# Optimization experiments

Measured on AMD Instinct MI355X. Metric: run time of the kernel, lower is better.

The kernel has to match this reference:

```python
import jax, jax.numpy as jnp
import numpy as np

DK = 8.0          # sqrt(in_dim) with in_dim = 64
BN_SCALE = 1.0 / np.float32(np.sqrt(1.0 + 1e-5))  # eval-mode BatchNorm3d at init (mean=0, var=1, gamma=1, beta=0)


def conv3d(x, w, b):
    # x: [B,Cin,D1,D2,D3], w: [Cout,Cin,3,3,3], stride 1, padding 1 == SAME
    y = jax.lax.conv_general_dilated(
        x, w, window_strides=(1, 1, 1), padding='SAME',
        dimension_numbers=('NCDHW', 'OIDHW', 'NCDHW'))
    return y + b[None, :, None, None, None]


def axial(qm, km, vm):
    # qm/km/vm: [B,C,S,L,M]; attention over L with keys along M-contraction.
    # scores[b,c,s,i,j] = sum_m (q/dk)[...,i,m] * k[...,j,m]  -> [B,C,S,L,L]
    s = jnp.einsum('bcsim,bcsjm->bcsij', qm / DK, km)
    # torch nn.Softmax(dim=1) applied to [N,L,L] normalizes over the FIRST L axis (i)
    a = jax.nn.softmax(s, axis=-2)
    return jnp.einsum('bcsij,bcsjm->bcsim', a, vm)


def setup_inputs() -> dict:
    key = jax.random.key(0)
    ks = jax.random.split(key, 5)
    B, C, H, W, D = 2, 64, 64, 64, 64
    x = jax.random.normal(ks[0], (B, C, H, W, D), jnp.float32)
    Wq = jax.random.normal(ks[1], (C, C, 3, 3, 3), jnp.float32) * 0.02
    Wk = jax.random.normal(ks[2], (C, C, 3, 3, 3), jnp.float32) * 0.02
    Wv = jax.random.normal(ks[3], (C, C, 3, 3, 3), jnp.float32) * 0.02
    Wc = jax.random.normal(ks[4], (C, 3 * C, 3, 3, 3), jnp.float32) * 0.02
    z = jnp.zeros((C,), jnp.float32)
    return {"x": x, "Wq": Wq, "bq": z, "Wk": Wk, "bk": z,
            "Wv": Wv, "bv": z, "Wc": Wc, "bc": z}


def reference(x, Wq, bq, Wk, bk, Wv, bv, Wc, bc):
    # projections (dropout is inactive at inference)
    q = conv3d(x, Wq, bq)
    k = conv3d(x, Wk, bk)
    v = conv3d(x, Wv, bv)
    P = jnp.transpose

    # ---- loop over D slices: attend over H (and over W in the transposed pass) ----
    pa = (0, 1, 4, 2, 3)        # [B,C,D,H,W]
    ava = axial(P(q, pa), P(k, pa), P(v, pa))          # [B,C,D,H,W]
    ava = P(ava, (0, 1, 3, 4, 2))                       # -> [B,C,H,W,D]
    pb = (0, 1, 4, 3, 2)        # [B,C,D,W,H]
    ava1 = axial(P(q, pb), P(k, pb), P(v, pb))          # [B,C,D,W,H]
    ava1 = P(ava1, (0, 1, 4, 3, 2))                     # -> [B,C,H,W,D]
    AVa = (ava + ava1) * 0.5

    # ---- loop over W slices: attend over H (and over D) ----
    pc = (0, 1, 3, 2, 4)        # [B,C,W,H,D]
    avb = axial(P(q, pc), P(k, pc), P(v, pc))           # [B,C,W,H,D]
    avb = P(avb, (0, 1, 3, 2, 4))                       # -> [B,C,H,W,D]
    pd = (0, 1, 3, 4, 2)        # [B,C,W,D,H]
    avb1 = axial(P(q, pd), P(k, pd), P(v, pd))          # [B,C,W,D,H]
    avb1 = P(avb1, (0, 1, 4, 2, 3))                     # -> [B,C,H,W,D]
    AVb = (avb + avb1) * 0.5

    # ---- loop over H slices: attend over W (and over D) ----
    avc = axial(q, k, v)                                 # [B,C,H,W,D]
    pe = (0, 1, 2, 4, 3)        # [B,C,H,D,W]
    avc1 = axial(P(q, pe), P(k, pe), P(v, pe))          # [B,C,H,D,W]
    avc1 = P(avc1, (0, 1, 2, 4, 3))                     # -> [B,C,H,W,D]
    AVc = (avc + avc1) * 0.5

    cat = jnp.concatenate([AVa, AVb, AVc], axis=1)      # [B,3C,H,W,D]
    y = jax.nn.relu(conv3d(cat, Wc, bc) * BN_SCALE)     # Conv_3x3x3: conv + BN(eval) + ReLU
    y = y * BN_SCALE                                    # outer BatchNorm3d (eval)
    return y + q
```

## Files before the change

### kernel.cpp

```cpp
#include <hip/hip_runtime.h>

typedef unsigned short u16;
typedef unsigned int u32;
typedef __attribute__((ext_vector_type(8))) __bf16 bf16x8;
typedef __attribute__((ext_vector_type(4))) float f32x4;
typedef __attribute__((ext_vector_type(4))) u16 u16x4;

#define VOL 262144
#define TSZ ((size_t)33554432)

__device__ __forceinline__ u16 f2bf(float f) {
  u32 u = __builtin_bit_cast(u32, f);
  u32 r = u + 0x7FFFu + ((u >> 16) & 1u);
  return (u16)(r >> 16);
}
__device__ __forceinline__ float bf2f(u16 h) {
  return __builtin_bit_cast(float, ((u32)h) << 16);
}
__device__ __forceinline__ bf16x8 ldsfrag(const u16* p) { return *(const bf16x8*)p; }

__device__ __forceinline__ void gload16(const u16* g, u16* l) {
  __builtin_amdgcn_global_load_lds(
      (const __attribute__((address_space(1))) u32*)g,
      (__attribute__((address_space(3))) u32*)l, 16, 0, 0);
}

__device__ __forceinline__ int swA(int row, int col) {
  return row * 64 + (col ^ (((row ^ (row >> 3)) & 7) << 3));
}

__global__ __launch_bounds__(256) void swz_qkv(const float* __restrict__ Wq,
    const float* __restrict__ Wk, const float* __restrict__ Wv, u16* __restrict__ out) {
  int idx = blockIdx.x * 256 + threadIdx.x;
  if (idx >= 54 * 12 * 64 * 8) return;
  int jj = idx & 7;
  int lane = (idx >> 3) & 63;
  int t = idx >> 9;
  int nf = t % 12, s = t / 12;
  int dh = s / 18, sub = s % 18;
  int dw = sub / 6, dd = (sub >> 1) % 3, c32 = sub & 1;
  int coutg = nf * 16 + (lane & 15);
  int cin = c32 * 32 + (lane >> 4) * 8 + jj;
  const float* W = (coutg < 64) ? Wq : ((coutg < 128) ? Wk : Wv);
  int c = coutg & 63;
  out[idx] = f2bf(W[(c * 64 + cin) * 27 + dh * 9 + dw * 3 + dd]);
}

__global__ __launch_bounds__(256) void swz_c(const float* __restrict__ Wc, u16* __restrict__ out) {
  int idx = blockIdx.x * 256 + threadIdx.x;
  if (idx >= 162 * 4 * 64 * 8) return;
  int jj = idx & 7;
  int lane = (idx >> 3) & 63;
  int nf = (idx >> 9) & 3;
  int s = idx >> 11;
  int dh = s / 54, rem = s % 54;
  int t = rem / 18, sub = rem % 18;
  int dw = sub / 6, dd = (sub >> 1) % 3, c32 = sub & 1;
  int cout = nf * 16 + (lane & 15);
  int cin = t * 64 + c32 * 32 + (lane >> 4) * 8 + jj;
  out[idx] = f2bf(Wc[(cout * 192 + cin) * 27 + dh * 9 + dw * 3 + dd]);
}

__global__ __launch_bounds__(256, 4) void xcvt(const float* __restrict__ x, u16* __restrict__ xcl) {
  __shared__ __align__(16) u16 tile[4096];
  int id = blockIdx.x;
  int b = id >> 12;
  int t = threadIdx.x;
  int c0 = (t & 31) * 2, d0 = (t >> 5) * 8;
  const float* p0 = x + (size_t)(b * 64 + c0) * VOL + (size_t)(id & 4095) * 64 + d0;
  float4 r00 = *(const float4*)p0;
  float4 r01 = *(const float4*)(p0 + 4);
  float4 r10 = *(const float4*)(p0 + VOL);
  float4 r11 = *(const float4*)(p0 + VOL + 4);
  float a0[8] = {r00.x, r00.y, r00.z, r00.w, r01.x, r01.y, r01.z, r01.w};
  float a1[8] = {r10.x, r10.y, r10.z, r10.w, r11.x, r11.y, r11.z, r11.w};
#pragma unroll
  for (int i = 0; i < 8; ++i) {
    int d = d0 + i;
    *(u32*)&tile[d * 64 + (c0 ^ ((d & 7) << 3))] =
        (u32)f2bf(a0[i]) | ((u32)f2bf(a1[i]) << 16);
  }
  __syncthreads();
  u16* dst = xcl + ((size_t)id << 12);
  *(uint4*)&dst[t * 16] = *(const uint4*)&tile[t * 16];
  *(uint4*)&dst[t * 16 + 8] = *(const uint4*)&tile[t * 16 + 8];
}

__global__ __launch_bounds__(256, 4) void repackA(const u16* __restrict__ src, u16* __restrict__ dst) {
  __shared__ __align__(16) u16 T[64 * 4 * 72];
  int j = blockIdx.x;
  int b = j >> 10, h = (j >> 4) & 63, d0 = (j & 15) * 4;
  int tid = threadIdx.x;
  int kk = d0 & 4;
#pragma unroll
  for (int k = 0; k < 8; ++k) {
    int chunk = tid + 256 * k;
    int row = chunk >> 3, woct = chunk & 7;
    int c = row >> 2, dd = row & 3;
    uint4 v = *(const uint4*)&src[(size_t)(b * 64 + c) * VOL + (size_t)(d0 + dd) * 4096 +
                                  h * 64 + woct * 8];
    union { uint4 u; u16 s[8]; } U; U.u = v;
    int d7 = kk + dd;
#pragma unroll
    for (int wi = 0; wi < 8; ++wi) {
      T[(woct * 8 + wi) * 288 + dd * 72 + (c ^ ((d7 ^ wi) << 3))] = U.s[wi];
    }
  }
  __syncthreads();
#pragma unroll
  for (int k = 0; k < 8; ++k) {
    int cn = tid + 256 * k;
    int w = cn >> 5, rem = cn & 31;
    int dd = rem >> 3, j8 = rem & 7;
    uint4 v = *(const uint4*)&T[w * 288 + dd * 72 + ((j8 ^ (w & 7)) << 3)];
    *(uint4*)&dst[(size_t)((b * 64 + h) * 64 + w) * 4096 + (d0 + dd) * 64 + j8 * 8] = v;
  }
}

__global__ __launch_bounds__(256, 4) void repackB(const u16* __restrict__ src, u16* __restrict__ dst) {
  __shared__ __align__(16) u16 T[4 * 64 * 72];
  int j = blockIdx.x;
  int b = j >> 10, h = (j >> 4) & 63, w0 = (j & 15) * 4;
  int tid = threadIdx.x;
#pragma unroll
  for (int k = 0; k < 8; ++k) {
    int chunk = tid + 256 * k;
    int row = chunk >> 3, doct = chunk & 7;
    int c = row >> 2, wi2 = row & 3;
    uint4 v = *(const uint4*)&src[(size_t)(b * 64 + c) * VOL + h * 4096 + (w0 + wi2) * 64 +
                                  doct * 8];
    union { uint4 u; u16 s[8]; } U; U.u = v;
#pragma unroll
    for (int di = 0; di < 8; ++di) {
      T[wi2 * 4608 + (doct * 8 + di) * 72 + (c ^ ((di ^ wi2) << 3))] = U.s[di];
    }
  }
  __syncthreads();
#pragma unroll
  for (int k = 0; k < 8; ++k) {
    int cn = tid + 256 * k;
    int wi2 = cn >> 9, rem = cn & 511;
    int d = rem >> 3, j8 = rem & 7;
    uint4 v = *(const uint4*)&T[wi2 * 4608 + d * 72 + ((j8 ^ wi2) << 3)];
    *(uint4*)&dst[(size_t)((b * 64 + h) * 64 + w0 + wi2) * 4096 + d * 64 + j8 * 8] = v;
  }
}

__global__ __launch_bounds__(512, 2) void conv_qkv(const u16* __restrict__ xcl,
    const u16* __restrict__ BQ, const float* __restrict__ bq, const float* __restrict__ bk,
    const float* __restrict__ bv, u16* __restrict__ qb, u16* __restrict__ kb,
    u16* __restrict__ vb) {
  __shared__ __align__(16) u16 xT[2 * 16896];
  int tid = threadIdx.x;
  int id = blockIdx.x;
  int lin = (id & 7) * 512 + (id >> 3);
  int b = lin >> 11, h = (lin >> 5) & 63, w0 = (lin & 31) * 2;
  int wave = tid >> 6, lane = tid & 63, r = lane & 15, g = lane >> 4;
  int mhalf = wave >> 2, nq = wave & 3;
  {
    int tl = tid >> 7, rs = (tid >> 6) & 1, ci = tid & 63;
    int off = tl * 4224 + rs * 65 * 64 + ci;
    xT[off] = 0;
    xT[16896 + off] = 0;
  }
  if (w0 == 0) {
    *(uint4*)&xT[64 + tid * 8] = uint4{0, 0, 0, 0};
    *(uint4*)&xT[16896 + 64 + tid * 8] = uint4{0, 0, 0, 0};
  }
  if (w0 == 62) {
    *(uint4*)&xT[3 * 4224 + 64 + tid * 8] = uint4{0, 0, 0, 0};
    *(uint4*)&xT[16896 + 3 * 4224 + 64 + tid * 8] = uint4{0, 0, 0, 0};
  }
  int tw = wave >> 1, half = wave & 1;
  int wws = w0 + tw - 1;
  bool doload = (unsigned)wws < 64u;

  f32x4 acc[4][3];
#pragma unroll
  for (int i = 0; i < 4; ++i)
#pragma unroll
    for (int j = 0; j < 3; ++j)
#pragma unroll
      for (int e = 0; e < 4; ++e) acc[i][j][e] = 0.0f;

  int dhlo = (h == 0) ? 1 : 0, dhhi = (h == 63) ? 1 : 2;
  if (doload) {
    int hh = h + dhlo - 1;
    const u16* gp = xcl + (((size_t)(b * 64 + hh) * 64 + wws) << 12) + (half << 11) + (lane << 3);
    u16* lp = &xT[tw * 4224 + 64 + half * 2048];
#pragma unroll
    for (int j = 0; j < 4; ++j) gload16(gp + j * 512, lp + j * 512);
  }
  int cur = 0;
  for (int dh = dhlo; dh <= dhhi; ++dh) {
    __syncthreads();
    if (dh < dhhi && doload) {
      int hh = h + dh;
      const u16* gp =
          xcl + (((size_t)(b * 64 + hh) * 64 + wws) << 12) + (half << 11) + (lane << 3);
      u16* lp = &xT[(cur ^ 1) * 16896 + tw * 4224 + 64 + half * 2048];
#pragma unroll
      for (int j = 0; j < 4; ++j) gload16(gp + j * 512, lp + j * 512);
    }
    const u16* Bbase = BQ + ((size_t)(dh * 18) * 12 + nq * 3) * 512 + (size_t)lane * 8;
    int bufE = cur * 16896;
    for (int sub = 0; sub < 18; ++sub) {
      int dw = sub / 6, dd = (sub >> 1) % 3, c32 = sub & 1;
      int colb = c32 * 32 + g * 8;
      int wwi = mhalf + dw;
      bf16x8 A[4];
#pragma unroll
      for (int l = 0; l < 4; ++l) {
        int dpos = l * 16 + r + dd;
        A[l] = ldsfrag(&xT[bufE + wwi * 4224 + dpos * 64 + (colb ^ (((dpos - 1) & 7) << 3))]);
      }
      const u16* Bp = Bbase + (size_t)sub * 12 * 512;
#pragma unroll
      for (int nf = 0; nf < 3; ++nf) {
        bf16x8 Bf = *(const bf16x8*)(Bp + nf * 512);
#pragma unroll
        for (int l = 0; l < 4; ++l)
          acc[l][nf] = __builtin_amdgcn_mfma_f32_16x16x32_bf16(A[l], Bf, acc[l][nf], 0, 0, 0);
      }
    }
    cur ^= 1;
  }
#pragma unroll
  for (int nf = 0; nf < 3; ++nf) {
    int coutg = (nq * 3 + nf) * 16 + r;
    int ten = coutg >> 6, c = coutg & 63;
    u16* dst = (ten == 0) ? qb : ((ten == 1) ? kb : vb);
    const float* bias = (ten == 0) ? bq : ((ten == 1) ? bk : bv);
    float bsv = bias[c];
#pragma unroll
    for (int l = 0; l < 4; ++l) {
      int d0 = l * 16 + g * 4;
      int idx = (b * 64 + c) * VOL + h * 4096 + (w0 + mhalf) * 64 + d0;
      u16x4 o;
#pragma unroll
      for (int jj = 0; jj < 4; ++jj) o[jj] = f2bf(acc[l][nf][jj] + bsv);
      *(u16x4*)(dst + idx) = o;
    }
  }
}

__global__ __launch_bounds__(256, 6) void ktranspose(const u16* __restrict__ src,
    u16* __restrict__ dst, int P, int Q) {
  __shared__ __align__(16) u16 tile[64 * 72];
  int tid = threadIdx.x;
  int id = blockIdx.x;
  int bc = id >> 6, t = id & 63;
  int qt = Q >> 6;
  int p0 = (t / qt) * 64, q0 = (t % qt) * 64;
  const u16* s = src + (size_t)bc * VOL;
  u16* d = dst + (size_t)bc * VOL;
#pragma unroll
  for (int it = 0; it < 2; ++it) {
    int c = tid + 256 * it;
    int i2 = c >> 3, sg = c & 7;
    *(uint4*)&tile[i2 * 72 + ((sg * 8) ^ (((i2 >> 3) & 7) << 3))] =
        *(const uint4*)&s[(size_t)(p0 + i2) * Q + q0 + sg * 8];
  }
  __syncthreads();
  int j = tid >> 2, ms = tid & 3;
  u16 vals[16];
#pragma unroll
  for (int ii = 0; ii < 16; ++ii) {
    int row = ms * 16 + ii;
    vals[ii] = tile[row * 72 + (j ^ (((row >> 3) & 7) << 3))];
  }
  uint4 o0, o1;
  o0.x = (u32)vals[0] | ((u32)vals[1] << 16);
  o0.y = (u32)vals[2] | ((u32)vals[3] << 16);
  o0.z = (u32)vals[4] | ((u32)vals[5] << 16);
  o0.w = (u32)vals[6] | ((u32)vals[7] << 16);
  o1.x = (u32)vals[8] | ((u32)vals[9] << 16);
  o1.y = (u32)vals[10] | ((u32)vals[11] << 16);
  o1.z = (u32)vals[12] | ((u32)vals[13] << 16);
  o1.w = (u32)vals[14] | ((u32)vals[15] << 16);
  size_t drow = (size_t)(q0 + j) * P + p0 + ms * 16;
  *(uint4*)&d[drow] = o0;
  *(uint4*)&d[drow + 8] = o1;
}

__global__ __launch_bounds__(256, 2) void attn_pair(const u16* __restrict__ q,
    const u16* __restrict__ k, const u16* __restrict__ v, u16* __restrict__ dst,
    int uStride, int sMul) {
  __shared__ __align__(16) u16 sm[6 * 4096];
  u16* LQ = sm;             u16* LK = sm + 4096;      u16* LV = sm + 2 * 4096;
  u16* LQT = sm + 3 * 4096; u16* LKT = sm + 4 * 4096; u16* LVT = sm + 5 * 4096;
  u16* A1 = LK;
  u16* A2 = LKT;
  int tid = threadIdx.x;
  int id = blockIdx.x;
  int bc = id >> 6, sidx = id & 63;
  size_t base = (size_t)bc * VOL + (size_t)sidx * sMul;
  int wave = tid >> 6, lane = tid & 63, r = lane & 15, g = lane >> 4;
  int pairid = tid >> 3, seg = tid & 7;
  int u0 = pairid * 2;
  const u16* srcs[3] = {q, k, v};
  u16* Ln_[3] = {LQ, LK, LV};
  u16* Lt_[3] = {LQT, LKT, LVT};
#pragma unroll
  for (int t3 = 0; t3 < 3; ++t3) {
    const u16* p = srcs[t3] + base + (size_t)u0 * uStride + seg * 8;
    uint4 ra = *(const uint4*)p;
    uint4 rb = *(const uint4*)(p + uStride);
    *(uint4*)&Ln_[t3][swA(u0, seg * 8)] = ra;
    *(uint4*)&Ln_[t3][swA(u0 + 1, seg * 8)] = rb;
    union { uint4 vv; u16 ss[8]; } Ua, Ub;
    Ua.vv = ra; Ub.vv = rb;
#pragma unroll
    for (int vi = 0; vi < 8; ++vi) {
      int vvx = seg * 8 + vi;
      *(u32*)&Lt_[t3][swA(vvx, u0)] = (u32)Ua.ss[vi] | ((u32)Ub.ss[vi] << 16);
    }
  }
  __syncthreads();
  int row0 = wave * 16;
  f32x4 s1[4], s2[4];
#pragma unroll
  for (int nf = 0; nf < 4; ++nf)
#pragma unroll
    for (int e = 0; e < 4; ++e) { s1[nf][e] = 0.f; s2[nf][e] = 0.f; }
#pragma unroll
  for (int ks = 0; ks < 2; ++ks) {
    int cb = ks * 32 + g * 8;
    bf16x8 aK = ldsfrag(&LK[swA(row0 + r, cb)]);
    bf16x8 aKT = ldsfrag(&LKT[swA(row0 + r, cb)]);
#pragma unroll
    for (int nf = 0; nf < 4; ++nf) {
      bf16x8 bQ = ldsfrag(&LQ[swA(nf * 16 + r, cb)]);
      bf16x8 bQT = ldsfrag(&LQT[swA(nf * 16 + r, cb)]);
      s1[nf] = __builtin_amdgcn_mfma_f32_16x16x32_bf16(aK, bQ, s1[nf], 0, 0, 0);
      s2[nf] = __builtin_amdgcn_mfma_f32_16x16x32_bf16(aKT, bQT, s2[nf], 0, 0, 0);
    }
  }
  __syncthreads();
#pragma unroll
  for (int m2 = 0; m2 < 2; ++m2) {
    f32x4* ss = m2 ? s2 : s1;
    u16* Adst = m2 ? A2 : A1;
#pragma unroll
    for (int jj = 0; jj < 4; ++jj) {
      float mx = fmaxf(fmaxf(ss[0][jj], ss[1][jj]), fmaxf(ss[2][jj], ss[3][jj]));
      mx = fmaxf(mx, __shfl_xor(mx, 1, 64));
      mx = fmaxf(mx, __shfl_xor(mx, 2, 64));
      mx = fmaxf(mx, __shfl_xor(mx, 4, 64));
      mx = fmaxf(mx, __shfl_xor(mx, 8, 64));
      float p0 = __expf((ss[0][jj] - mx) * 0.125f);
      float p1 = __expf((ss[1][jj] - mx) * 0.125f);
      float p2 = __expf((ss[2][jj] - mx) * 0.125f);
      float p3 = __expf((ss[3][jj] - mx) * 0.125f);
      float sum = p0 + p1 + p2 + p3;
      sum += __shfl_xor(sum, 1, 64);
      sum += __shfl_xor(sum, 2, 64);
      sum += __shfl_xor(sum, 4, 64);
      sum += __shfl_xor(sum, 8, 64);
      float inv = 1.0f / sum;
      ss[0][jj] = p0 * inv; ss[1][jj] = p1 * inv; ss[2][jj] = p2 * inv; ss[3][jj] = p3 * inv;
    }
    int j0 = row0 + g * 4;
#pragma unroll
    for (int nf = 0; nf < 4; ++nf) {
      int i = nf * 16 + r;
      int a0 = swA(i, j0);
      *(u32*)&Adst[a0]     = (u32)f2bf(ss[nf][0]) | ((u32)f2bf(ss[nf][1]) << 16);
      *(u32*)&Adst[a0 + 2] = (u32)f2bf(ss[nf][2]) | ((u32)f2bf(ss[nf][3]) << 16);
    }
  }
  __syncthreads();
  f32x4 o[4];
#pragma unroll
  for (int nf = 0; nf < 4; ++nf)
#pragma unroll
    for (int e = 0; e < 4; ++e) o[nf][e] = 0.f;
#pragma unroll
  for (int ks = 0; ks < 2; ++ks) {
    int cb = ks * 32 + g * 8;
    bf16x8 aA = ldsfrag(&A1[swA(row0 + r, cb)]);
    bf16x8 aV = ldsfrag(&LV[swA(row0 + r, cb)]);
#pragma unroll
    for (int nf = 0; nf < 4; ++nf) {
      bf16x8 bVT = ldsfrag(&LVT[swA(nf * 16 + r, cb)]);
      bf16x8 bA2 = ldsfrag(&A2[swA(nf * 16 + r, cb)]);
      o[nf] = __builtin_amdgcn_mfma_f32_16x16x32_bf16(aA, bVT, o[nf], 0, 0, 0);
      o[nf] = __builtin_amdgcn_mfma_f32_16x16x32_bf16(aV, bA2, o[nf], 0, 0, 0);
    }
  }
#pragma unroll
  for (int nf = 0; nf < 4; ++nf) {
    int vv = nf * 16 + r;
#pragma unroll
    for (int jj = 0; jj < 4; ++jj) {
      int u = row0 + g * 4 + jj;
      dst[base + (size_t)u * uStride + vv] = f2bf(o[nf][jj] * 0.5f);
    }
  }
}

__global__ __launch_bounds__(512, 2) void conv_final(const u16* __restrict__ avcl,
    const u16* __restrict__ BCw, const float* __restrict__ bcb,
    const u16* __restrict__ qb, float* __restrict__ out) {
  __shared__ __align__(16) u16 xT[6 * 4224];
  int tid = threadIdx.x;
  int id = blockIdx.x;
  int lin = (id & 7) * 256 + (id >> 3);
  int b = lin >> 10, h = (lin >> 4) & 63, w0 = (lin & 15) * 4;
  int wave = tid >> 6, lane = tid & 63, r = lane & 15, g = lane >> 4;
  int mw = wave >> 1, nw = wave & 1;
  for (int z = tid; z < 768; z += 512) {
    int tl = z >> 7, rs = (z >> 6) & 1, ci = z & 63;
    xT[tl * 4224 + rs * 65 * 64 + ci] = 0;
  }
  if (w0 == 0) *(uint4*)&xT[64 + tid * 8] = uint4{0, 0, 0, 0};
  if (w0 == 60) *(uint4*)&xT[5 * 4224 + 64 + tid * 8] = uint4{0, 0, 0, 0};

  int tw1 = wave >> 1, hf1 = wave & 1;
  int tw2 = 4 + (wave >> 1), hf2 = wave & 1;
  int ww1 = w0 + tw1 - 1, ww2 = w0 + tw2 - 1;
  bool dl1 = (unsigned)ww1 < 64u;
  bool dl2 = (wave < 4) && ((unsigned)ww2 < 64u);

  f32x4 acc[4][2];
#pragma unroll
  for (int i = 0; i < 4; ++i)
#pragma unroll
    for (int j = 0; j < 2; ++j)
#pragma unroll
      for (int e = 0; e < 4; ++e) acc[i][j][e] = 0.f;

  for (int dh = 0; dh < 3; ++dh) {
    int hh = h + dh - 1;
    if ((unsigned)hh >= 64u) continue;
    for (int t = 0; t < 3; ++t) {
      __syncthreads();
      const u16* tbase = avcl + (size_t)t * TSZ;
      if (dl1) {
        const u16* gp = tbase + (((size_t)(b * 64 + hh) * 64 + ww1) << 12) + (hf1 << 11) + (lane << 3);
        u16* lp = &xT[tw1 * 4224 + 64 + hf1 * 2048];
#pragma unroll
        for (int j = 0; j < 4; ++j) gload16(gp + j * 512, lp + j * 512);
      }
      if (dl2) {
        const u16* gp = tbase + (((size_t)(b * 64 + hh) * 64 + ww2) << 12) + (hf2 << 11) + (lane << 3);
        u16* lp = &xT[tw2 * 4224 + 64 + hf2 * 2048];
#pragma unroll
        for (int j = 0; j < 4; ++j) gload16(gp + j * 512, lp + j * 512);
      }
      __syncthreads();
      const u16* Bbase = BCw + ((size_t)((dh * 3 + t) * 18) * 4 + nw * 2) * 512 + (size_t)lane * 8;
      for (int sub = 0; sub < 18; ++sub) {
        int dw = sub / 6, dd = (sub >> 1) % 3, c32 = sub & 1;
        int colb = c32 * 32 + g * 8;
        int wwi = mw + dw;
        bf16x8 A[4];
#pragma unroll
        for (int dq = 0; dq < 4; ++dq) {
          int dpos = dq * 16 + r + dd;
          A[dq] = ldsfrag(&xT[wwi * 4224 + dpos * 64 + (colb ^ (((dpos - 1) & 7) << 3))]);
        }
        const u16* Bp = Bbase + (size_t)sub * 4 * 512;
#pragma unroll
        for (int nf = 0; nf < 2; ++nf) {
          bf16x8 Bf = *(const bf16x8*)(Bp + nf * 512);
#pragma unroll
          for (int dq = 0; dq < 4; ++dq)
            acc[dq][nf] = __builtin_amdgcn_mfma_f32_16x16x32_bf16(A[dq], Bf, acc[dq][nf], 0, 0, 0);
        }
      }
    }
  }
  const float S = 0.9999950000374997f;
#pragma unroll
  for (int nf = 0; nf < 2; ++nf) {
    int cout = (nw * 2 + nf) * 16 + r;
    float bsv = bcb[cout];
#pragma unroll
    for (int dq = 0; dq < 4; ++dq) {
      int d0 = dq * 16 + g * 4;
      int idx = (b * 64 + cout) * VOL + h * 4096 + (w0 + mw) * 64 + d0;
      u16x4 qv = *(const u16x4*)(qb + idx);
      float4 ov;
      float t0 = (acc[dq][nf][0] + bsv) * S; t0 = t0 > 0.f ? t0 : 0.f; ov.x = t0 * S + bf2f(qv[0]);
      float t1 = (acc[dq][nf][1] + bsv) * S; t1 = t1 > 0.f ? t1 : 0.f; ov.y = t1 * S + bf2f(qv[1]);
      float t2 = (acc[dq][nf][2] + bsv) * S; t2 = t2 > 0.f ? t2 : 0.f; ov.z = t2 * S + bf2f(qv[2]);
      float t3 = (acc[dq][nf][3] + bsv) * S; t3 = t3 > 0.f ? t3 : 0.f; ov.w = t3 * S + bf2f(qv[3]);
      *(float4*)(out + idx) = ov;
    }
  }
}

extern "C" void kernel_launch(void* const* d_in, const int* in_sizes, int n_in,
                              void* d_out, int out_size, void* d_ws, size_t ws_size,
                              hipStream_t stream) {
  const float* x  = (const float*)d_in[0];
  const float* Wq = (const float*)d_in[1];
  const float* bq = (const float*)d_in[2];
  const float* Wk = (const float*)d_in[3];
  const float* bk = (const float*)d_in[4];
  const float* Wv = (const float*)d_in[5];
  const float* bv = (const float*)d_in[6];
  const float* Wc = (const float*)d_in[7];
  const float* bc = (const float*)d_in[8];
  float* out = (float*)d_out;
  u16* ws = (u16*)d_ws;
  u16* qb = ws;
  u16* kb = ws + TSZ;
  u16* vb = ws + 2 * TSZ;
  u16* qT = ws + 3 * TSZ;
  u16* kT = ws + 4 * TSZ;
  u16* vT = ws + 5 * TSZ;
  u16* X  = ws + 6 * TSZ;
  u16* BQ = ws + 7 * TSZ;
  u16* BC = BQ + 331776;
  u16* avcl = qT;

  swz_qkv<<<1296, 256, 0, stream>>>(Wq, Wk, Wv, BQ);
  swz_c<<<1296, 256, 0, stream>>>(Wc, BC);
  xcvt<<<8192, 256, 0, stream>>>(x, X);
  conv_qkv<<<4096, 512, 0, stream>>>(X, BQ, bq, bk, bv, qb, kb, vb);
  ktranspose<<<8192, 256, 0, stream>>>(qb, qT, 4096, 64);
  ktranspose<<<8192, 256, 0, stream>>>(kb, kT, 4096, 64);
  ktranspose<<<8192, 256, 0, stream>>>(vb, vT, 4096, 64);
  attn_pair<<<8192, 256, 0, stream>>>(qT, kT, vT, X, 64, 4096);
  repackA<<<2048, 256, 0, stream>>>(X, avcl);
  attn_pair<<<8192, 256, 0, stream>>>(qb, kb, vb, X, 4096, 64);
  repackB<<<2048, 256, 0, stream>>>(X, avcl + TSZ);
  attn_pair<<<8192, 256, 0, stream>>>(qb, kb, vb, X, 64, 4096);
  repackB<<<2048, 256, 0, stream>>>(X, avcl + 2 * TSZ);
  conv_final<<<2048, 512, 0, stream>>>(avcl, BC, bc, qb, out);
}
```

Before: 1.060 ms.

## Double-buffer LDS tiles in final conv to overlap loads with MFMA

The final 3x3x3 conv kernel now keeps two LDS input buffers. It prefetches the next (dh, t) slab with global_load_lds while MFMAs run on the current one, so each step needs one barrier instead of two. The out-of-range h rows are now skipped by computing loop bounds up front instead of continuing inside the loop. In exchange, LDS per block roughly doubles to about 100 KB. That likely stops two 512-thread blocks from sharing a CU, which lowers occupancy and the latency hiding that came from running two blocks.

```diff
diff --git a/kernel.cpp b/kernel.cpp
--- a/kernel.cpp
+++ b/kernel.cpp
@@ -402,20 +402,25 @@
 __global__ __launch_bounds__(512, 2) void conv_final(const u16* __restrict__ avcl,
     const u16* __restrict__ BCw, const float* __restrict__ bcb,
     const u16* __restrict__ qb, float* __restrict__ out) {
-  __shared__ __align__(16) u16 xT[6 * 4224];
+  __shared__ __align__(16) u16 xT[2 * 25344];
   int tid = threadIdx.x;
   int id = blockIdx.x;
   int lin = (id & 7) * 256 + (id >> 3);
   int b = lin >> 10, h = (lin >> 4) & 63, w0 = (lin & 15) * 4;
   int wave = tid >> 6, lane = tid & 63, r = lane & 15, g = lane >> 4;
   int mw = wave >> 1, nw = wave & 1;
-  for (int z = tid; z < 768; z += 512) {
+  for (int z = tid; z < 1536; z += 512) {
     int tl = z >> 7, rs = (z >> 6) & 1, ci = z & 63;
     xT[tl * 4224 + rs * 65 * 64 + ci] = 0;
   }
-  if (w0 == 0) *(uint4*)&xT[64 + tid * 8] = uint4{0, 0, 0, 0};
-  if (w0 == 60) *(uint4*)&xT[5 * 4224 + 64 + tid * 8] = uint4{0, 0, 0, 0};
-
+  if (w0 == 0) {
+    *(uint4*)&xT[64 + tid * 8] = uint4{0, 0, 0, 0};
+    *(uint4*)&xT[25344 + 64 + tid * 8] = uint4{0, 0, 0, 0};
+  }
+  if (w0 == 60) {
+    *(uint4*)&xT[5 * 4224 + 64 + tid * 8] = uint4{0, 0, 0, 0};
+    *(uint4*)&xT[25344 + 5 * 4224 + 64 + tid * 8] = uint4{0, 0, 0, 0};
+  }
   int tw1 = wave >> 1, hf1 = wave & 1;
   int tw2 = 4 + (wave >> 1), hf2 = wave & 1;
   int ww1 = w0 + tw1 - 1, ww2 = w0 + tw2 - 1;
@@ -430,46 +435,57 @@
 #pragma unroll
       for (int e = 0; e < 4; ++e) acc[i][j][e] = 0.f;
 
-  for (int dh = 0; dh < 3; ++dh) {
+  int dhlo = (h == 0) ? 1 : 0, dhhi = (h == 63) ? 1 : 2;
+  int np = (dhhi - dhlo + 1) * 3;
+
+  auto stage = [&](int bufE, int dh, int t) {
     int hh = h + dh - 1;
-    if ((unsigned)hh >= 64u) continue;
-    for (int t = 0; t < 3; ++t) {
-      __syncthreads();
-      const u16* tbase = avcl + (size_t)t * TSZ;
-      if (dl1) {
-        const u16* gp = tbase + (((size_t)(b * 64 + hh) * 64 + ww1) << 12) + (hf1 << 11) + (lane << 3);
-        u16* lp = &xT[tw1 * 4224 + 64 + hf1 * 2048];
-#pragma unroll
-        for (int j = 0; j < 4; ++j) gload16(gp + j * 512, lp + j * 512);
+    const u16* tbase = avcl + (size_t)t * TSZ;
+    if (dl1) {
+      const u16* gp = tbase + (((size_t)(b * 64 + hh) * 64 + ww1) << 12) + (hf1 << 11) + (lane << 3);
+      u16* lp = &xT[bufE + tw1 * 4224 + 64 + hf1 * 2048];
+#pragma unroll
+      for (int j = 0; j < 4; ++j) gload16(gp + j * 512, lp + j * 512);
+    }
+    if (dl2) {
+      const u16* gp = tbase + (((size_t)(b * 64 + hh) * 64 + ww2) << 12) + (hf2 << 11) + (lane << 3);
+      u16* lp = &xT[bufE + tw2 * 4224 + 64 + hf2 * 2048];
+#pragma unroll
+      for (int j = 0; j < 4; ++j) gload16(gp + j * 512, lp + j * 512);
+    }
+  };
+
+  stage(0, dhlo, 0);
+  int cur = 0;
+  for (int p = 0; p < np; ++p) {
+    __syncthreads();
+    if (p + 1 < np) {
+      int pn = p + 1;
+      stage((cur ^ 1) * 25344, dhlo + pn / 3, pn % 3);
+    }
+    int dh = dhlo + p / 3, t = p % 3;
+    const u16* Bbase = BCw + ((size_t)((dh * 3 + t) * 18) * 4 + nw * 2) * 512 + (size_t)lane * 8;
+    int bufE = cur * 25344;
+    for (int sub = 0; sub < 18; ++sub) {
+      int dw = sub / 6, dd = (sub >> 1) % 3, c32 = sub & 1;
+      int colb = c32 * 32 + g * 8;
+      int wwi = mw + dw;
+      bf16x8 A[4];
+#pragma unroll
+      for (int dq = 0; dq < 4; ++dq) {
+        int dpos = dq * 16 + r + dd;
+        A[dq] = ldsfrag(&xT[bufE + wwi * 4224 + dpos * 64 + (colb ^ (((dpos - 1) & 7) << 3))]);
       }
-      if (dl2) {
-        const u16* gp = tbase + (((size_t)(b * 64 + hh) * 64 + ww2) << 12) + (hf2 << 11) + (lane << 3);
-        u16* lp = &xT[tw2 * 4224 + 64 + hf2 * 2048];
-#pragma unroll
-        for (int j = 0; j < 4; ++j) gload16(gp + j * 512, lp + j * 512);
+      const u16* Bp = Bbase + (size_t)sub * 4 * 512;
+#pragma unroll
+      for (int nf = 0; nf < 2; ++nf) {
+        bf16x8 Bf = *(const bf16x8*)(Bp + nf * 512);
+#pragma unroll
+        for (int dq = 0; dq < 4; ++dq)
+          acc[dq][nf] = __builtin_amdgcn_mfma_f32_16x16x32_bf16(A[dq], Bf, acc[dq][nf], 0, 0, 0);
       }
-      __syncthreads();
-      const u16* Bbase = BCw + ((size_t)((dh * 3 + t) * 18) * 4 + nw * 2) * 512 + (size_t)lane * 8;
-      for (int sub = 0; sub < 18; ++sub) {
-        int dw = sub / 6, dd = (sub >> 1) % 3, c32 = sub & 1;
-        int colb = c32 * 32 + g * 8;
-        int wwi = mw + dw;
-        bf16x8 A[4];
-#pragma unroll
-        for (int dq = 0; dq < 4; ++dq) {
-          int dpos = dq * 16 + r + dd;
-          A[dq] = ldsfrag(&xT[wwi * 4224 + dpos * 64 + (colb ^ (((dpos - 1) & 7) << 3))]);
-        }
-        const u16* Bp = Bbase + (size_t)sub * 4 * 512;
-#pragma unroll
-        for (int nf = 0; nf < 2; ++nf) {
-          bf16x8 Bf = *(const bf16x8*)(Bp + nf * 512);
-#pragma unroll
-          for (int dq = 0; dq < 4; ++dq)
-            acc[dq][nf] = __builtin_amdgcn_mfma_f32_16x16x32_bf16(A[dq], Bf, acc[dq][nf], 0, 0, 0);
-        }
-      }
-    }
+    }
+    cur ^= 1;
   }
   const float S = 0.9999950000374997f;
 #pragma unroll
```

Measured after the change: 1.185 ms. 11.8% more time.
